# Kernel tuning notes

Measured on AMD Instinct MI355X. Metric: run time of the kernel, lower is better.

Reference implementation:

```python
import jax, jax.numpy as jnp
import numpy as np

KSIZE = 11
SIGMA = 1.5
CHANNELS = 1


def _gaussian_kernel(size=KSIZE, sigma=SIGMA, channels=CHANNELS):
    coords = jnp.arange(size, dtype=jnp.float32) - size // 2
    g = jnp.exp(-coords ** 2 / (2.0 * sigma ** 2))
    g = g / g.sum()
    k2d = jnp.outer(g, g)  # [k, k]
    # depthwise kernel, OIHW with I=1 per group
    return jnp.broadcast_to(k2d, (channels, 1, size, size))


def _dwconv(x, k):
    pad = KSIZE // 2
    return jax.lax.conv_general_dilated(
        x, k, window_strides=(1, 1), padding=[(pad, pad), (pad, pad)],
        dimension_numbers=('NCHW', 'OIHW', 'NCHW'),
        feature_group_count=CHANNELS)


def setup_inputs() -> dict:
    key = jax.random.key(0)
    k1, k2 = jax.random.split(key)
    x_hat = jax.random.normal(k1, (64, 1, 512, 512), dtype=jnp.float32)
    x = jax.random.normal(k2, (64, 1, 512, 512), dtype=jnp.float32)
    kernel = _gaussian_kernel()
    return {"x_hat": x_hat, "x": x, "kernel": kernel}


def reference(x_hat, x, kernel):
    C1, C2 = 0.01 ** 2, 0.03 ** 2
    # shift [-1,1] -> [0,1]
    a = (x + 1.0) / 2.0          # 'x' in _ssim
    b = (x_hat + 1.0) / 2.0      # 'y' in _ssim
    mu_x = _dwconv(a, kernel)
    mu_y = _dwconv(b, kernel)
    mu_x2 = mu_x ** 2
    mu_y2 = mu_y ** 2
    mu_xy = mu_x * mu_y
    sig_x = _dwconv(a * a, kernel) - mu_x2
    sig_y = _dwconv(b * b, kernel) - mu_y2
    sig_xy = _dwconv(a * b, kernel) - mu_xy
    num = (2.0 * mu_xy + C1) * (2.0 * sig_xy + C2)
    den = (mu_x2 + mu_y2 + C1) * (sig_x + sig_y + C2)
    ssim = (num / (den + 1e-08)).mean()
    return 1.0 - ssim
```

## Files before the change

### kernel.cpp

```cpp
#include <hip/hip_runtime.h>

typedef float v2f __attribute__((ext_vector_type(2)));

#define IMG_W 512
#define IMG_H 512
#define RH    64
#define BW    128
#define KS    11
#define KR    5
#define OFFP  9
#define LROWP (OFFP + BW + OFFP)
#define ROWS  (RH + 2 * KR)
#define NPH   77

struct Pf { float ax, ay, bx, by, lx, lb, rx, rb; };

__global__ __launch_bounds__(64, 2)
void ssim_main(const float* __restrict__ xhat,
               const float* __restrict__ x,
               const float* __restrict__ kern,
               float* __restrict__ accum)
{
    __shared__ float lds[2][2 * LROWP];

    const int lane  = threadIdx.x;
    const int band  = blockIdx.x & 3;
    const int strip = (blockIdx.x >> 2) & 7;
    const int img   = blockIdx.x >> 5;
    const int base  = band * BW;
    const int R0    = strip * RH;
    const float* xp = x    + (size_t)img * (IMG_W * IMG_H);
    const float* hp = xhat + (size_t)img * (IMG_W * IMG_H);

    float g[KS];
    {
        const float inv = rsqrtf(kern[5 * KS + 5]);
        #pragma unroll
        for (int i = 0; i < KS; ++i) g[i] = kern[5 * KS + i] * inv;
    }

    const int  c0   = lane << 1;
    const bool lh   = lane < KR;
    const bool rhn  = lane >= 64 - KR;
    const int  lcol = base - KR + lane;
    const int  rcol = base + BW + (lane - (64 - KR));
    const int  lidx = OFFP - KR + lane;
    const int  ridx = OFFP + BW + (lane - (64 - KR));

    auto load_row = [&](int rr) -> Pf {
        Pf p = {0.f,0.f,0.f,0.f,0.f,0.f,0.f,0.f};
        const int ri = R0 - KR + rr;
        if (ri >= 0 && ri < IMG_H) {
            const size_t ro = (size_t)ri * IMG_W;
            const float2 vx = *(const float2*)(xp + ro + base + c0);
            const float2 vh = *(const float2*)(hp + ro + base + c0);
            p.ax = fmaf(vx.x, 0.5f, 0.5f);  p.ay = fmaf(vx.y, 0.5f, 0.5f);
            p.bx = fmaf(vh.x, 0.5f, 0.5f);  p.by = fmaf(vh.y, 0.5f, 0.5f);
            if (lh && lcol >= 0) {
                p.lx = fmaf(xp[ro + lcol], 0.5f, 0.5f);
                p.lb = fmaf(hp[ro + lcol], 0.5f, 0.5f);
            }
            if (rhn && rcol < IMG_W) {
                p.rx = fmaf(xp[ro + rcol], 0.5f, 0.5f);
                p.rb = fmaf(hp[ro + rcol], 0.5f, 0.5f);
            }
        }
        return p;
    };

    v2f   h01r[KS][2];
    v2f   h23r[KS][2];
    float h4r [KS][2];
    float acc = 0.f;
    const float C1 = 1e-4f, C2 = 9e-4f;

    Pf pfA = load_row(0);
    Pf pfB = load_row(1);
    float* bufA = lds[0];
    float* bufB = lds[1];

    #pragma unroll 1
    for (int rblk = 0; rblk < NPH; rblk += KS) {
        #pragma unroll
        for (int p = 0; p < KS; ++p) {
            const int rr = rblk + p;
            if (rr < ROWS) {
                constexpr bool evenp = true;
                Pf&    cur = ((p & 1) == 0) ? pfA : pfB;
                float* buf = ((p & 1) == 0) ? bufA : bufB;

                *(float2*)&buf[2 * (OFFP + c0)]     = make_float2(cur.ax, cur.bx);
                *(float2*)&buf[2 * (OFFP + c0) + 2] = make_float2(cur.ay, cur.by);
                if (lh)  *(float2*)&buf[2 * lidx] = make_float2(cur.lx, cur.lb);
                if (rhn) *(float2*)&buf[2 * ridx] = make_float2(cur.rx, cur.rb);
                __asm__ __volatile__("s_waitcnt lgkmcnt(0)" ::: "memory");

                if (rr + 2 < ROWS) cur = load_row(rr + 2);

                const float4* q = (const float4*)buf;
                const int qb = lane + (OFFP - KR) / 2;
                float4 w[6];
                #pragma unroll
                for (int j = 0; j < 6; ++j) w[j] = q[qb + j];

                v2f h01[2] = {{0.f,0.f},{0.f,0.f}};
                v2f h23[2] = {{0.f,0.f},{0.f,0.f}};
                float h4[2] = {0.f, 0.f};
                #pragma unroll
                for (int t = 0; t < KS + 1; ++t) {
                    v2f ab;
                    ab.x = (t & 1) ? w[t >> 1].z : w[t >> 1].x;
                    ab.y = (t & 1) ? w[t >> 1].w : w[t >> 1].y;
                    const v2f  ab2 = ab * ab;
                    const float pab = ab.x * ab.y;
                    if (t < KS) {
                        const v2f wv = {g[t], g[t]};
                        h01[0] = __builtin_elementwise_fma(ab,  wv, h01[0]);
                        h23[0] = __builtin_elementwise_fma(ab2, wv, h23[0]);
                        h4[0]  = fmaf(pab, g[t], h4[0]);
                    }
                    if (t > 0) {
                        const v2f wv = {g[t - 1], g[t - 1]};
                        h01[1] = __builtin_elementwise_fma(ab,  wv, h01[1]);
                        h23[1] = __builtin_elementwise_fma(ab2, wv, h23[1]);
                        h4[1]  = fmaf(pab, g[t - 1], h4[1]);
                    }
                }
                #pragma unroll
                for (int c = 0; c < 2; ++c) {
                    h01r[p][c] = h01[c];
                    h23r[p][c] = h23[c];
                    h4r [p][c] = h4[c];
                }

                if (rr >= 2 * KR) {
                    v2f v01[2] = {{0.f,0.f},{0.f,0.f}};
                    v2f v23[2] = {{0.f,0.f},{0.f,0.f}};
                    float v4[2] = {0.f, 0.f};
                    #pragma unroll
                    for (int t = 0; t < KS; ++t) {
                        const int slot = (p + 1 + t) % KS;
                        const v2f wv = {g[t], g[t]};
                        #pragma unroll
                        for (int c = 0; c < 2; ++c) {
                            v01[c] = __builtin_elementwise_fma(h01r[slot][c], wv, v01[c]);
                            v23[c] = __builtin_elementwise_fma(h23r[slot][c], wv, v23[c]);
                            v4[c]  = fmaf(h4r[slot][c], g[t], v4[c]);
                        }
                    }
                    #pragma unroll
                    for (int c = 0; c < 2; ++c) {
                        const float mux  = v01[c].x, muy = v01[c].y;
                        const float mux2 = mux * mux;
                        const float muy2 = muy * muy;
                        const float muxy = mux * muy;
                        const float sx   = v23[c].x - mux2;
                        const float sy   = v23[c].y - muy2;
                        const float sxy  = v4[c]    - muxy;
                        const float num  = (2.f * muxy + C1) * (2.f * sxy + C2);
                        const float den  = (mux2 + muy2 + C1) * (sx + sy + C2);
                        acc = fmaf(num, __builtin_amdgcn_rcpf(den + 1e-8f), acc);
                    }
                }
            }
        }
        { Pf t = pfA; pfA = pfB; pfB = t; }
        { float* t = bufA; bufA = bufB; bufB = t; }
    }

    #pragma unroll
    for (int o = 32; o > 0; o >>= 1) acc += __shfl_down(acc, o, 64);
    if (lane == 0) atomicAdd(accum, acc);
}

__global__ void ssim_final(const float* __restrict__ accum,
                           float* __restrict__ out)
{
    out[0] = 1.0f - accum[0] * (1.0f / (64.0f * 512.0f * 512.0f));
}

extern "C" void kernel_launch(void* const* d_in, const int* in_sizes, int n_in,
                              void* d_out, int out_size, void* d_ws, size_t ws_size,
                              hipStream_t stream) {
    const float* xhat = (const float*)d_in[0];
    const float* xin  = (const float*)d_in[1];
    const float* kern = (const float*)d_in[2];
    float* out = (float*)d_out;
    float* ws  = (float*)d_ws;

    const int nimg = in_sizes[0] / (IMG_W * IMG_H);
    const int nblk = nimg * (IMG_H / RH) * (IMG_W / BW);

    hipMemsetAsync(ws, 0, sizeof(float), stream);
    ssim_main<<<nblk, 64, 0, stream>>>(xhat, xin, kern, ws);
    ssim_final<<<1, 1, 0, stream>>>(ws, out);
}
```

Before: 234.9 us.

## Halve strip height and defer the 0.5 shift until after the prefetch loads

Strip height drops from 64 to 32 rows, doubling the block count to add parallelism, at the cost of more vertical halo recomputation per output row (42 vs 74 rows processed per 32/64 outputs). Prefetched rows are now held raw, with out-of-bounds padding of -1 so it maps to 0 after the shift, and the fma affine shift moves to the LDS store. This is meant to let the global loads issue before the LDS waitcnt and stay in flight across the compute. The LDS buffer is also explicitly 16-byte aligned.

Result: no change. 231.9 us (-1.3%).

```diff
diff --git a/kernel.cpp b/kernel.cpp
--- a/kernel.cpp
+++ b/kernel.cpp
@@ -4,14 +4,14 @@
 
 #define IMG_W 512
 #define IMG_H 512
-#define RH    64
+#define RH    32
 #define BW    128
 #define KS    11
 #define KR    5
 #define OFFP  9
 #define LROWP (OFFP + BW + OFFP)
 #define ROWS  (RH + 2 * KR)
-#define NPH   77
+#define NPH   44
 
 struct Pf { float ax, ay, bx, by, lx, lb, rx, rb; };
 
@@ -21,12 +21,12 @@
                const float* __restrict__ kern,
                float* __restrict__ accum)
 {
-    __shared__ float lds[2][2 * LROWP];
+    __shared__ __align__(16) float lds[2][2 * LROWP];
 
     const int lane  = threadIdx.x;
     const int band  = blockIdx.x & 3;
-    const int strip = (blockIdx.x >> 2) & 7;
-    const int img   = blockIdx.x >> 5;
+    const int strip = (blockIdx.x >> 2) & 15;
+    const int img   = blockIdx.x >> 6;
     const int base  = band * BW;
     const int R0    = strip * RH;
     const float* xp = x    + (size_t)img * (IMG_W * IMG_H);
@@ -47,22 +47,22 @@
     const int  lidx = OFFP - KR + lane;
     const int  ridx = OFFP + BW + (lane - (64 - KR));
 
-    auto load_row = [&](int rr) -> Pf {
-        Pf p = {0.f,0.f,0.f,0.f,0.f,0.f,0.f,0.f};
+    auto load_raw = [&](int rr) -> Pf {
+        Pf p = {-1.f,-1.f,-1.f,-1.f,-1.f,-1.f,-1.f,-1.f};
         const int ri = R0 - KR + rr;
         if (ri >= 0 && ri < IMG_H) {
             const size_t ro = (size_t)ri * IMG_W;
             const float2 vx = *(const float2*)(xp + ro + base + c0);
             const float2 vh = *(const float2*)(hp + ro + base + c0);
-            p.ax = fmaf(vx.x, 0.5f, 0.5f);  p.ay = fmaf(vx.y, 0.5f, 0.5f);
-            p.bx = fmaf(vh.x, 0.5f, 0.5f);  p.by = fmaf(vh.y, 0.5f, 0.5f);
+            p.ax = vx.x;  p.ay = vx.y;
+            p.bx = vh.x;  p.by = vh.y;
             if (lh && lcol >= 0) {
-                p.lx = fmaf(xp[ro + lcol], 0.5f, 0.5f);
-                p.lb = fmaf(hp[ro + lcol], 0.5f, 0.5f);
+                p.lx = xp[ro + lcol];
+                p.lb = hp[ro + lcol];
             }
             if (rhn && rcol < IMG_W) {
-                p.rx = fmaf(xp[ro + rcol], 0.5f, 0.5f);
-                p.rb = fmaf(hp[ro + rcol], 0.5f, 0.5f);
+                p.rx = xp[ro + rcol];
+                p.rb = hp[ro + rcol];
             }
         }
         return p;
@@ -74,8 +74,8 @@
     float acc = 0.f;
     const float C1 = 1e-4f, C2 = 9e-4f;
 
-    Pf pfA = load_row(0);
-    Pf pfB = load_row(1);
+    Pf pfA = load_raw(0);
+    Pf pfB = load_raw(1);
     float* bufA = lds[0];
     float* bufB = lds[1];
 
@@ -85,23 +85,28 @@
         for (int p = 0; p < KS; ++p) {
             const int rr = rblk + p;
             if (rr < ROWS) {
-                constexpr bool evenp = true;
                 Pf&    cur = ((p & 1) == 0) ? pfA : pfB;
                 float* buf = ((p & 1) == 0) ? bufA : bufB;
 
-                *(float2*)&buf[2 * (OFFP + c0)]     = make_float2(cur.ax, cur.bx);
-                *(float2*)&buf[2 * (OFFP + c0) + 2] = make_float2(cur.ay, cur.by);
-                if (lh)  *(float2*)&buf[2 * lidx] = make_float2(cur.lx, cur.lb);
-                if (rhn) *(float2*)&buf[2 * ridx] = make_float2(cur.rx, cur.rb);
+                *(float2*)&buf[2 * (OFFP + c0)] =
+                    make_float2(fmaf(cur.ax, 0.5f, 0.5f), fmaf(cur.bx, 0.5f, 0.5f));
+                *(float2*)&buf[2 * (OFFP + c0) + 2] =
+                    make_float2(fmaf(cur.ay, 0.5f, 0.5f), fmaf(cur.by, 0.5f, 0.5f));
+                if (lh)  *(float2*)&buf[2 * lidx] =
+                    make_float2(fmaf(cur.lx, 0.5f, 0.5f), fmaf(cur.lb, 0.5f, 0.5f));
+                if (rhn) *(float2*)&buf[2 * ridx] =
+                    make_float2(fmaf(cur.rx, 0.5f, 0.5f), fmaf(cur.rb, 0.5f, 0.5f));
+
+                const bool hasNext = (rr + 2 < ROWS);
+                Pf nxt;
+                if (hasNext) nxt = load_raw(rr + 2);
+
                 __asm__ __volatile__("s_waitcnt lgkmcnt(0)" ::: "memory");
 
-                if (rr + 2 < ROWS) cur = load_row(rr + 2);
-
                 const float4* q = (const float4*)buf;
-                const int qb = lane + (OFFP - KR) / 2;
                 float4 w[6];
                 #pragma unroll
-                for (int j = 0; j < 6; ++j) w[j] = q[qb + j];
+                for (int j = 0; j < 6; ++j) w[j] = q[lane + 2 + j];
 
                 v2f h01[2] = {{0.f,0.f},{0.f,0.f}};
                 v2f h23[2] = {{0.f,0.f},{0.f,0.f}};
@@ -162,6 +167,8 @@
                         acc = fmaf(num, __builtin_amdgcn_rcpf(den + 1e-8f), acc);
                     }
                 }
+
+                if (hasNext) cur = nxt;
             }
         }
         { Pf t = pfA; pfA = pfB; pfB = t; }
```
